# Kernel tuning notes

Hardware: AMD Instinct MI355X
Metric: run time of the kernel (lower is better)

## Reference

```python
import jax, jax.numpy as jnp
import numpy as np

H_MAX = 0.05
TIME_LEN = 5  # t = linspace(0, 1, 5); uniform segments of length 0.25
N_STEPS = int(np.ceil(0.25 / H_MAX))  # Euler steps per segment = 5 (matches torch ode_solve)


def setup_inputs() -> dict:
    key = jax.random.key(0)
    k1, k2, k3, k4, k5 = jax.random.split(key, 5)
    bs, d, hidden = 1024, 1024, 2048
    z0 = jax.random.normal(k1, (bs, d), dtype=jnp.float32)
    t = jnp.linspace(0.0, 1.0, TIME_LEN).astype(jnp.float32)
    # MLP ODEF params: f(z, t) = tanh([z, t] @ W1 + b1) @ W2 + b2
    s1 = 1.0 / np.sqrt(d + 1)
    s2 = 1.0 / np.sqrt(hidden)
    W1 = jax.random.uniform(k2, (d + 1, hidden), jnp.float32, -s1, s1)
    b1 = jax.random.uniform(k3, (hidden,), jnp.float32, -s1, s1)
    W2 = jax.random.uniform(k4, (hidden, d), jnp.float32, -s2, s2)
    b2 = jax.random.uniform(k5, (d,), jnp.float32, -s2, s2)
    return {"z0": z0, "t": t, "W1": W1, "b1": b1, "W2": W2, "b2": b2}


def _f(z, t_scalar, W1, b1, W2, b2):
    # z: [bs, d]; t_scalar broadcast as an extra input feature
    bs = z.shape[0]
    zt = jnp.concatenate([z, jnp.full((bs, 1), t_scalar, dtype=z.dtype)], axis=1)
    h = jnp.tanh(zt @ W1 + b1)
    return h @ W2 + b2


def _ode_solve(z0, t0, t1, W1, b1, W2, b2):
    # Euler: z <- z + h * f(z, t), N_STEPS fixed steps (h_max = 0.05)
    h = (t1 - t0) / N_STEPS

    def step(carry, _):
        z, t = carry
        z = z + h * _f(z, t, W1, b1, W2, b2)
        return (z, t + h), None

    (z, _), _ = jax.lax.scan(step, (z0, t0), None, length=N_STEPS)
    return z


def reference(z0, t, W1, b1, W2, b2):
    # NeuralODE.forward with return_whole_sequence=False: returns z at final time point.
    z = z0
    for i in range(TIME_LEN - 1):  # small fixed loop over time checkpoints
        z = _ode_solve(z, t[i], t[i + 1], W1, b1, W2, b2)
    return z
```

## Files before the change

kernel.cpp:

```cpp
#include <hip/hip_runtime.h>
#include <cstdint>
#include <cstddef>


typedef __bf16 bf16x8 __attribute__((ext_vector_type(8)));
typedef float f32x4 __attribute__((ext_vector_type(4)));

#define WAITV(N) asm volatile("s_waitcnt vmcnt(" #N ") lgkmcnt(0)" ::: "memory")
#define BARRIER() asm volatile("s_barrier" ::: "memory")
#define SEP() asm volatile("" ::: "memory")

__device__ __forceinline__ unsigned short f2bf(float f) {
  union { float f; unsigned u; } v; v.f = f;
  unsigned r = v.u + 0x7fffu + ((v.u >> 16) & 1u);
  return (unsigned short)(r >> 16);
}

__device__ __forceinline__ float fast_tanh(float x) {
  float e = __builtin_amdgcn_exp2f(x * 2.8853900817779268f);
  return 1.0f - 2.0f * __builtin_amdgcn_rcpf(1.0f + e);
}

__global__ void prep_all(const float* __restrict__ W1,
                         const float* __restrict__ W2,
                         unsigned short* __restrict__ W1T,
                         unsigned short* __restrict__ W2T,
                         const float* __restrict__ z0,
                         float* __restrict__ zf,
                         unsigned short* __restrict__ zbf,
                         float* __restrict__ w1l) {
  __shared__ float tile[32][33];
  const int b = blockIdx.x;
  const int tid = threadIdx.x;
  const int tx = tid & 31, ty = tid >> 5;
  if (b < 4096) {
    const bool w1 = (b < 2048);
    const float* in = w1 ? W1 : W2;
    unsigned short* out = w1 ? W1T : W2T;
    const int rows = w1 ? 1024 : 2048;
    const int cols = w1 ? 2048 : 1024;
    const int bb = w1 ? b : b - 2048;
    const int c0 = w1 ? (bb & 63) * 32 : (bb & 31) * 32;
    const int r0 = w1 ? (bb >> 6) * 32 : (bb >> 5) * 32;
#pragma unroll
    for (int j = 0; j < 32; j += 8)
      tile[ty + j][tx] = in[(size_t)(r0 + ty + j) * cols + (c0 + tx)];
    __syncthreads();
#pragma unroll
    for (int j = 0; j < 32; j += 8)
      out[(size_t)(c0 + ty + j) * rows + (r0 + tx)] = f2bf(tile[tx][ty + j]);
  } else {
    const int i = (b - 4096) * 256 + tid;
    float v = z0[i];
    zf[i] = v;
    zbf[i] = f2bf(v);
    if (i < 2048) w1l[i] = W1[(size_t)1024 * 2048 + i];
  }
}

__device__ __forceinline__ void stage64(const unsigned short* __restrict__ g,
                                        size_t ld, int row0, int k0,
                                        unsigned short* lp, int tid) {
  int r = tid >> 3;
  int c = (tid & 7) ^ (r & 7);
  __builtin_amdgcn_global_load_lds(
      (const __attribute__((address_space(1))) void*)(
          g + (size_t)(row0 + r) * ld + k0 + c * 8),
      (__attribute__((address_space(3))) void*)(lp + tid * 8), 16, 0, 0);
}

__device__ __forceinline__ bf16x8 frag_ld(const unsigned short* lp, int row,
                                          int chunk_logical, int x) {
  return *(const bf16x8*)(lp + row * 64 + ((chunk_logical ^ x) << 3));
}

__global__ __launch_bounds__(512, 1) void gemm1_kernel(
    const unsigned short* __restrict__ Zb,
    const unsigned short* __restrict__ W1T,
    unsigned short* __restrict__ H,
    const float* __restrict__ b1, const float* __restrict__ w1l, float tval) {
  __shared__ __align__(16) unsigned short lds[73728];
  const int tid = threadIdx.x;
  const int lane = tid & 63, wid = tid >> 6;
  const int l15 = lane & 15, q = lane >> 4, x = l15 & 7;
  const int bid = blockIdx.x;
  const int xcd = bid & 7, loc = bid >> 3;
  const int mt = (loc & 3) | ((xcd & 3) << 2);
  const int nt = (loc >> 2) | ((xcd >> 2) << 3);
  const int m0 = mt * 64, n0 = nt * 128;

  unsigned short* const buf0 = lds;
  unsigned short* const buf1 = lds + 24576;
  unsigned short* const buf2 = lds + 49152;

  f32x4 acc[2][2] = {};

  auto stage_tile = [&](int t, unsigned short* p) {
    int k = t * 128;
    stage64(Zb, 1024, m0, k, p, tid);
    stage64(Zb, 1024, m0, k + 64, p + 4096, tid);
    stage64(W1T, 1024, n0, k, p + 8192, tid);
    stage64(W1T, 1024, n0 + 64, k, p + 12288, tid);
    stage64(W1T, 1024, n0, k + 64, p + 16384, tid);
    stage64(W1T, 1024, n0 + 64, k + 64, p + 20480, tid);
  };
  auto compute = [&](const unsigned short* p) {
    const unsigned short* A0 = p + (wid & 1) * 2048;
    const unsigned short* B0 = p + 8192 + (wid >> 1) * 2048;
#pragma unroll
    for (int kk = 0; kk < 4; ++kk) {
      const unsigned short* A = A0 + (kk >> 1) * 4096;
      const unsigned short* B = B0 + (kk >> 1) * 8192;
      const int cb = ((kk & 1) << 2) + q;
      bf16x8 a[2], bb[2];
#pragma unroll
      for (int im = 0; im < 2; ++im)
        a[im] = frag_ld(A, im * 16 + l15, cb, x);
#pragma unroll
      for (int jn = 0; jn < 2; ++jn)
        bb[jn] = frag_ld(B, jn * 16 + l15, cb, x);
#pragma unroll
      for (int im = 0; im < 2; ++im)
#pragma unroll
        for (int jn = 0; jn < 2; ++jn)
          acc[im][jn] = __builtin_amdgcn_mfma_f32_16x16x32_bf16(
              a[im], bb[jn], acc[im][jn], 0, 0, 0);
    }
  };

#define STEP(t, pc, pn) \
  WAITV(6);             \
  BARRIER();            \
  stage_tile((t) + 2, pn); \
  compute(pc)

  stage_tile(0, buf0);
  SEP();
  stage_tile(1, buf1);

  STEP(0, buf0, buf2);
  STEP(1, buf1, buf0);
  STEP(2, buf2, buf1);
  STEP(3, buf0, buf2);
  STEP(4, buf1, buf0);
  STEP(5, buf2, buf1);
  WAITV(6);
  BARRIER();
  compute(buf0);
  WAITV(0);
  BARRIER();
  compute(buf1);
#undef STEP

#pragma unroll
  for (int jn = 0; jn < 2; ++jn) {
    int col = n0 + (wid >> 1) * 32 + jn * 16 + l15;
    float bb = b1[col] + tval * w1l[col];
#pragma unroll
    for (int im = 0; im < 2; ++im) {
      int rowb = m0 + (wid & 1) * 32 + im * 16 + q * 4;
#pragma unroll
      for (int r = 0; r < 4; ++r)
        H[(size_t)(rowb + r) * 2048 + col] =
            f2bf(fast_tanh(acc[im][jn][r] + bb));
    }
  }
}

__global__ __launch_bounds__(512, 1) void gemm2_kernel(
    const unsigned short* __restrict__ Hb,
    const unsigned short* __restrict__ W2T,
    const float* __restrict__ b2,
    const float* __restrict__ zf,
    float* __restrict__ outf,
    unsigned short* __restrict__ zbf,
    float h) {
  __shared__ __align__(16) unsigned short lds[49152];
  const int tid = threadIdx.x;
  const int lane = tid & 63, wid = tid >> 6;
  const int l15 = lane & 15, q = lane >> 4, x = l15 & 7;
  const int kh = wid >> 2, mh = (wid >> 1) & 1, nh = wid & 1;
  const int bid = blockIdx.x;
  const int xcd = bid & 7, loc = bid >> 3;
  const int mt = (loc & 3) | ((xcd & 3) << 2);
  const int nt = (loc >> 2) | ((xcd >> 2) << 3);
  const int m0 = mt * 64, n0 = nt * 64;

  unsigned short* const buf0 = lds;
  unsigned short* const buf1 = lds + 16384;
  unsigned short* const buf2 = lds + 32768;

  f32x4 acc[2][2] = {};

  auto stage_tile = [&](int t, unsigned short* p) {
    int k = t * 64;
    stage64(Hb, 2048, m0, k, p, tid);
    stage64(Hb, 2048, m0, k + 1024, p + 4096, tid);
    stage64(W2T, 2048, n0, k, p + 8192, tid);
    stage64(W2T, 2048, n0, k + 1024, p + 12288, tid);
  };
  auto compute = [&](const unsigned short* p) {
    const unsigned short* A = p + kh * 4096 + mh * 2048;
    const unsigned short* B = p + 8192 + kh * 4096 + nh * 2048;
#pragma unroll
    for (int kk = 0; kk < 2; ++kk) {
      bf16x8 a[2], bb[2];
#pragma unroll
      for (int im = 0; im < 2; ++im)
        a[im] = frag_ld(A, im * 16 + l15, (kk << 2) + q, x);
#pragma unroll
      for (int jn = 0; jn < 2; ++jn)
        bb[jn] = frag_ld(B, jn * 16 + l15, (kk << 2) + q, x);
#pragma unroll
      for (int im = 0; im < 2; ++im)
#pragma unroll
        for (int jn = 0; jn < 2; ++jn)
          acc[im][jn] = __builtin_amdgcn_mfma_f32_16x16x32_bf16(
              a[im], bb[jn], acc[im][jn], 0, 0, 0);
    }
  };

#define STEP(t, pc, pn) \
  WAITV(4);             \
  BARRIER();            \
  stage_tile((t) + 2, pn); \
  compute(pc)

  stage_tile(0, buf0);
  SEP();
  stage_tile(1, buf1);

  STEP(0, buf0, buf2);
  STEP(1, buf1, buf0);
  STEP(2, buf2, buf1);
  STEP(3, buf0, buf2);
  STEP(4, buf1, buf0);
  STEP(5, buf2, buf1);
  STEP(6, buf0, buf2);
  STEP(7, buf1, buf0);
  STEP(8, buf2, buf1);
  STEP(9, buf0, buf2);
  STEP(10, buf1, buf0);
  STEP(11, buf2, buf1);
  STEP(12, buf0, buf2);
  STEP(13, buf1, buf0);
  WAITV(4);
  BARRIER();
  compute(buf2);
  WAITV(0);
  BARRIER();
  compute(buf0);
#undef STEP

  __syncthreads();
  float* red = (float*)lds;
  const int region = (mh * 2 + nh) * 1056;
  if (kh == 1) {
#pragma unroll
    for (int im = 0; im < 2; ++im)
#pragma unroll
      for (int jn = 0; jn < 2; ++jn) {
        int c = jn * 16 + l15;
#pragma unroll
        for (int r = 0; r < 4; ++r)
          red[region + (im * 16 + q * 4 + r) * 33 + c] = acc[im][jn][r];
      }
  }
  __syncthreads();
  if (kh == 0) {
#pragma unroll
    for (int jn = 0; jn < 2; ++jn) {
      int coll = nh * 32 + jn * 16 + l15;
      int col = n0 + coll;
      float bb = b2[col];
#pragma unroll
      for (int im = 0; im < 2; ++im) {
        int rowl = im * 16 + q * 4;
#pragma unroll
        for (int r = 0; r < 4; ++r) {
          float s = acc[im][jn][r] +
                    red[region + (rowl + r) * 33 + jn * 16 + l15];
          size_t gidx = (size_t)(m0 + mh * 32 + rowl + r) * 1024 + col;
          float zv = zf[gidx] + h * (s + bb);
          outf[gidx] = zv;
          zbf[gidx] = f2bf(zv);
        }
      }
    }
  }
}

extern "C" void kernel_launch(void* const* d_in, const int* in_sizes, int n_in,
                              void* d_out, int out_size, void* d_ws,
                              size_t ws_size, hipStream_t stream) {
  const float* z0 = (const float*)d_in[0];
  const float* W1 = (const float*)d_in[2];
  const float* b1 = (const float*)d_in[3];
  const float* W2 = (const float*)d_in[4];
  const float* b2 = (const float*)d_in[5];
  float* out = (float*)d_out;

  char* ws = (char*)d_ws;
  unsigned short* W1T = (unsigned short*)(ws + 0);
  unsigned short* W2T = (unsigned short*)(ws + (4u << 20));
  unsigned short* zbf = (unsigned short*)(ws + (8u << 20));
  unsigned short* Hbf = (unsigned short*)(ws + (10u << 20));
  float* zf = (float*)(ws + (14u << 20));
  float* w1l = (float*)(ws + (18u << 20));

  prep_all<<<8192, 256, 0, stream>>>(W1, W2, W1T, W2T, z0, zf, zbf, w1l);

  const float h = 0.05f;
  for (int seg = 0; seg < 4; ++seg) {
    float tcur = 0.25f * (float)seg;
    for (int j = 0; j < 5; ++j) {
      gemm1_kernel<<<256, 512, 0, stream>>>(zbf, W1T, Hbf, b1, w1l, tcur);
      bool last = (seg == 3 && j == 4);
      float* outf = last ? out : zf;
      gemm2_kernel<<<256, 512, 0, stream>>>(Hbf, W2T, b2, zf, outf, zbf, h);
      tcur += h;
    }
  }
}
```

Measured before the change: 436.9 us.

## Store activations in MFMA-fragment order and load A operands directly from global

The bf16 copies of z and of the hidden activation H are now written in a pre-swizzled layout that matches the per-lane MFMA A-fragment order. Each GEMM then reads A fragments straight from global memory into registers instead of staging them through LDS. Only the weight tiles go through the LDS pipeline, so the LDS footprint and the staging traffic per step both shrink. The cost is scattered epilogue stores and global-load latency on the A path, which is only partly covered by the existing prefetch barrier scheme.

```diff
diff --git a/kernel.cpp b/kernel.cpp
--- a/kernel.cpp
+++ b/kernel.cpp
@@ -9,6 +9,7 @@
 #define WAITV(N) asm volatile("s_waitcnt vmcnt(" #N ") lgkmcnt(0)" ::: "memory")
 #define BARRIER() asm volatile("s_barrier" ::: "memory")
 #define SEP() asm volatile("" ::: "memory")
+#define MFMA(a, b, c) __builtin_amdgcn_mfma_f32_16x16x32_bf16(a, b, c, 0, 0, 0)
 
 __device__ __forceinline__ unsigned short f2bf(float f) {
   union { float f; unsigned u; } v; v.f = f;
@@ -53,7 +54,11 @@
     const int i = (b - 4096) * 256 + tid;
     float v = z0[i];
     zf[i] = v;
-    zbf[i] = f2bf(v);
+    const int R = i >> 10, C = i & 1023;
+    const int off = ((R >> 6) * 16 + (C >> 6)) * 4096 + ((R >> 5) & 1) * 2048 +
+                    ((C >> 5) & 1) * 1024 + ((R >> 4) & 1) * 512 +
+                    ((C >> 3) & 3) * 128 + (R & 15) * 8 + (C & 7);
+    zbf[off] = f2bf(v);
     if (i < 2048) w1l[i] = W1[(size_t)1024 * 2048 + i];
   }
 }
@@ -79,90 +84,101 @@
     const unsigned short* __restrict__ W1T,
     unsigned short* __restrict__ H,
     const float* __restrict__ b1, const float* __restrict__ w1l, float tval) {
-  __shared__ __align__(16) unsigned short lds[73728];
+  __shared__ __align__(16) unsigned short lds[24576];
   const int tid = threadIdx.x;
   const int lane = tid & 63, wid = tid >> 6;
   const int l15 = lane & 15, q = lane >> 4, x = l15 & 7;
+  const int mh = wid & 1, nq = wid >> 1;
   const int bid = blockIdx.x;
   const int xcd = bid & 7, loc = bid >> 3;
   const int mt = (loc & 3) | ((xcd & 3) << 2);
   const int nt = (loc >> 2) | ((xcd >> 2) << 3);
-  const int m0 = mt * 64, n0 = nt * 128;
+  const int n0 = nt * 128;
 
   unsigned short* const buf0 = lds;
-  unsigned short* const buf1 = lds + 24576;
-  unsigned short* const buf2 = lds + 49152;
+  unsigned short* const buf1 = lds + 8192;
+  unsigned short* const buf2 = lds + 16384;
 
   f32x4 acc[2][2] = {};
 
+  const unsigned short* const Af = Zb + (size_t)(mt * 16) * 4096 + mh * 2048 + lane * 8;
+
   auto stage_tile = [&](int t, unsigned short* p) {
-    int k = t * 128;
-    stage64(Zb, 1024, m0, k, p, tid);
-    stage64(Zb, 1024, m0, k + 64, p + 4096, tid);
-    stage64(W1T, 1024, n0, k, p + 8192, tid);
-    stage64(W1T, 1024, n0 + 64, k, p + 12288, tid);
-    stage64(W1T, 1024, n0, k + 64, p + 16384, tid);
-    stage64(W1T, 1024, n0 + 64, k + 64, p + 20480, tid);
+    int k = t * 64;
+    stage64(W1T, 1024, n0, k, p, tid);
+    stage64(W1T, 1024, n0 + 64, k, p + 4096, tid);
   };
-  auto compute = [&](const unsigned short* p) {
-    const unsigned short* A0 = p + (wid & 1) * 2048;
-    const unsigned short* B0 = p + 8192 + (wid >> 1) * 2048;
-#pragma unroll
-    for (int kk = 0; kk < 4; ++kk) {
-      const unsigned short* A = A0 + (kk >> 1) * 4096;
-      const unsigned short* B = B0 + (kk >> 1) * 8192;
-      const int cb = ((kk & 1) << 2) + q;
-      bf16x8 a[2], bb[2];
-#pragma unroll
-      for (int im = 0; im < 2; ++im)
-        a[im] = frag_ld(A, im * 16 + l15, cb, x);
-#pragma unroll
-      for (int jn = 0; jn < 2; ++jn)
-        bb[jn] = frag_ld(B, jn * 16 + l15, cb, x);
-#pragma unroll
-      for (int im = 0; im < 2; ++im)
-#pragma unroll
-        for (int jn = 0; jn < 2; ++jn)
-          acc[im][jn] = __builtin_amdgcn_mfma_f32_16x16x32_bf16(
-              a[im], bb[jn], acc[im][jn], 0, 0, 0);
-    }
+  auto compute = [&](const unsigned short* p, bf16x8 a00, bf16x8 a01,
+                     bf16x8 a10, bf16x8 a11) {
+    const unsigned short* B = p + nq * 2048;
+    bf16x8 b0 = frag_ld(B, l15, q, x);
+    bf16x8 b1v = frag_ld(B, 16 + l15, q, x);
+    acc[0][0] = MFMA(a00, b0, acc[0][0]);
+    acc[0][1] = MFMA(a00, b1v, acc[0][1]);
+    acc[1][0] = MFMA(a01, b0, acc[1][0]);
+    acc[1][1] = MFMA(a01, b1v, acc[1][1]);
+    bf16x8 b2 = frag_ld(B, l15, 4 + q, x);
+    bf16x8 b3 = frag_ld(B, 16 + l15, 4 + q, x);
+    acc[0][0] = MFMA(a10, b2, acc[0][0]);
+    acc[0][1] = MFMA(a10, b3, acc[0][1]);
+    acc[1][0] = MFMA(a11, b2, acc[1][0]);
+    acc[1][1] = MFMA(a11, b3, acc[1][1]);
   };
 
-#define STEP(t, pc, pn) \
-  WAITV(6);             \
-  BARRIER();            \
-  stage_tile((t) + 2, pn); \
-  compute(pc)
+#define STEP(t, pc, pn, W)                              \
+  {                                                     \
+    WAITV(W);                                           \
+    BARRIER();                                          \
+    const unsigned short* Ab = Af + (t) * 4096;         \
+    bf16x8 a00 = *(const bf16x8*)(Ab);                  \
+    bf16x8 a01 = *(const bf16x8*)(Ab + 512);            \
+    bf16x8 a10 = *(const bf16x8*)(Ab + 1024);           \
+    bf16x8 a11 = *(const bf16x8*)(Ab + 1536);           \
+    SEP();                                              \
+    if ((t) < 14) stage_tile((t) + 2, pn);              \
+    compute(pc, a00, a01, a10, a11);                    \
+  }
 
   stage_tile(0, buf0);
   SEP();
   stage_tile(1, buf1);
 
-  STEP(0, buf0, buf2);
-  STEP(1, buf1, buf0);
-  STEP(2, buf2, buf1);
-  STEP(3, buf0, buf2);
-  STEP(4, buf1, buf0);
-  STEP(5, buf2, buf1);
-  WAITV(6);
-  BARRIER();
-  compute(buf0);
-  WAITV(0);
-  BARRIER();
-  compute(buf1);
+  STEP(0, buf0, buf2, 2);
+  STEP(1, buf1, buf0, 2);
+  STEP(2, buf2, buf1, 2);
+  STEP(3, buf0, buf2, 2);
+  STEP(4, buf1, buf0, 2);
+  STEP(5, buf2, buf1, 2);
+  STEP(6, buf0, buf2, 2);
+  STEP(7, buf1, buf0, 2);
+  STEP(8, buf2, buf1, 2);
+  STEP(9, buf0, buf2, 2);
+  STEP(10, buf1, buf0, 2);
+  STEP(11, buf2, buf1, 2);
+  STEP(12, buf0, buf2, 2);
+  STEP(13, buf1, buf0, 2);
+  STEP(14, buf2, buf1, 2);
+  STEP(15, buf0, buf1, 0);
 #undef STEP
 
-#pragma unroll
-  for (int jn = 0; jn < 2; ++jn) {
-    int col = n0 + (wid >> 1) * 32 + jn * 16 + l15;
-    float bb = b1[col] + tval * w1l[col];
-#pragma unroll
-    for (int im = 0; im < 2; ++im) {
-      int rowb = m0 + (wid & 1) * 32 + im * 16 + q * 4;
-#pragma unroll
-      for (int r = 0; r < 4; ++r)
-        H[(size_t)(rowb + r) * 2048 + col] =
-            f2bf(fast_tanh(acc[im][jn][r] + bb));
+  {
+    const int laneoff = (l15 >> 3) * 128 + q * 32 + (l15 & 7);
+#pragma unroll
+    for (int jn = 0; jn < 2; ++jn) {
+      const int colb = n0 + nq * 32 + jn * 16;
+      const int col = colb + l15;
+      const float bb = b1[col] + tval * w1l[col];
+      const int kh2 = colb >> 10;
+      const int c10 = colb & 1023;
+      const int t2 = c10 >> 6;
+      const int ckb = (c10 >> 3) & 7;
+      const int fb = ((mt * 2 + kh2) * 16 + t2) * 4096 + mh * 2048 +
+                     (ckb >> 2) * 1024 + (ckb & 3) * 128 + laneoff;
+#pragma unroll
+      for (int im = 0; im < 2; ++im)
+#pragma unroll
+        for (int r = 0; r < 4; ++r)
+          H[fb + im * 512 + r * 8] = f2bf(fast_tanh(acc[im][jn][r] + bb));
     }
   }
 }
@@ -175,7 +191,7 @@
     float* __restrict__ outf,
     unsigned short* __restrict__ zbf,
     float h) {
-  __shared__ __align__(16) unsigned short lds[49152];
+  __shared__ __align__(16) unsigned short lds[24576];
   const int tid = threadIdx.x;
   const int lane = tid & 63, wid = tid >> 6;
   const int l15 = lane & 15, q = lane >> 4, x = l15 & 7;
@@ -187,69 +203,70 @@
   const int m0 = mt * 64, n0 = nt * 64;
 
   unsigned short* const buf0 = lds;
-  unsigned short* const buf1 = lds + 16384;
-  unsigned short* const buf2 = lds + 32768;
+  unsigned short* const buf1 = lds + 8192;
+  unsigned short* const buf2 = lds + 16384;
 
   f32x4 acc[2][2] = {};
+
+  const unsigned short* const Af =
+      Hb + (size_t)((mt * 2 + kh) * 16) * 4096 + mh * 2048 + lane * 8;
 
   auto stage_tile = [&](int t, unsigned short* p) {
     int k = t * 64;
-    stage64(Hb, 2048, m0, k, p, tid);
-    stage64(Hb, 2048, m0, k + 1024, p + 4096, tid);
-    stage64(W2T, 2048, n0, k, p + 8192, tid);
-    stage64(W2T, 2048, n0, k + 1024, p + 12288, tid);
+    stage64(W2T, 2048, n0, k, p, tid);
+    stage64(W2T, 2048, n0, k + 1024, p + 4096, tid);
   };
-  auto compute = [&](const unsigned short* p) {
-    const unsigned short* A = p + kh * 4096 + mh * 2048;
-    const unsigned short* B = p + 8192 + kh * 4096 + nh * 2048;
-#pragma unroll
-    for (int kk = 0; kk < 2; ++kk) {
-      bf16x8 a[2], bb[2];
-#pragma unroll
-      for (int im = 0; im < 2; ++im)
-        a[im] = frag_ld(A, im * 16 + l15, (kk << 2) + q, x);
-#pragma unroll
-      for (int jn = 0; jn < 2; ++jn)
-        bb[jn] = frag_ld(B, jn * 16 + l15, (kk << 2) + q, x);
-#pragma unroll
-      for (int im = 0; im < 2; ++im)
-#pragma unroll
-        for (int jn = 0; jn < 2; ++jn)
-          acc[im][jn] = __builtin_amdgcn_mfma_f32_16x16x32_bf16(
-              a[im], bb[jn], acc[im][jn], 0, 0, 0);
-    }
+  auto compute = [&](const unsigned short* p, bf16x8 a00, bf16x8 a01,
+                     bf16x8 a10, bf16x8 a11) {
+    const unsigned short* B = p + kh * 4096 + nh * 2048;
+    bf16x8 b0 = frag_ld(B, l15, q, x);
+    bf16x8 b1v = frag_ld(B, 16 + l15, q, x);
+    acc[0][0] = MFMA(a00, b0, acc[0][0]);
+    acc[0][1] = MFMA(a00, b1v, acc[0][1]);
+    acc[1][0] = MFMA(a01, b0, acc[1][0]);
+    acc[1][1] = MFMA(a01, b1v, acc[1][1]);
+    bf16x8 b2 = frag_ld(B, l15, 4 + q, x);
+    bf16x8 b3 = frag_ld(B, 16 + l15, 4 + q, x);
+    acc[0][0] = MFMA(a10, b2, acc[0][0]);
+    acc[0][1] = MFMA(a10, b3, acc[0][1]);
+    acc[1][0] = MFMA(a11, b2, acc[1][0]);
+    acc[1][1] = MFMA(a11, b3, acc[1][1]);
   };
 
-#define STEP(t, pc, pn) \
-  WAITV(4);             \
-  BARRIER();            \
-  stage_tile((t) + 2, pn); \
-  compute(pc)
+#define STEP(t, pc, pn, W)                              \
+  {                                                     \
+    WAITV(W);                                           \
+    BARRIER();                                          \
+    const unsigned short* Ab = Af + (t) * 4096;         \
+    bf16x8 a00 = *(const bf16x8*)(Ab);                  \
+    bf16x8 a01 = *(const bf16x8*)(Ab + 512);            \
+    bf16x8 a10 = *(const bf16x8*)(Ab + 1024);           \
+    bf16x8 a11 = *(const bf16x8*)(Ab + 1536);           \
+    SEP();                                              \
+    if ((t) < 14) stage_tile((t) + 2, pn);              \
+    compute(pc, a00, a01, a10, a11);                    \
+  }
 
   stage_tile(0, buf0);
   SEP();
   stage_tile(1, buf1);
 
-  STEP(0, buf0, buf2);
-  STEP(1, buf1, buf0);
-  STEP(2, buf2, buf1);
-  STEP(3, buf0, buf2);
-  STEP(4, buf1, buf0);
-  STEP(5, buf2, buf1);
-  STEP(6, buf0, buf2);
-  STEP(7, buf1, buf0);
-  STEP(8, buf2, buf1);
-  STEP(9, buf0, buf2);
-  STEP(10, buf1, buf0);
-  STEP(11, buf2, buf1);
-  STEP(12, buf0, buf2);
-  STEP(13, buf1, buf0);
-  WAITV(4);
-  BARRIER();
-  compute(buf2);
-  WAITV(0);
-  BARRIER();
-  compute(buf0);
+  STEP(0, buf0, buf2, 2);
+  STEP(1, buf1, buf0, 2);
+  STEP(2, buf2, buf1, 2);
+  STEP(3, buf0, buf2, 2);
+  STEP(4, buf1, buf0, 2);
+  STEP(5, buf2, buf1, 2);
+  STEP(6, buf0, buf2, 2);
+  STEP(7, buf1, buf0, 2);
+  STEP(8, buf2, buf1, 2);
+  STEP(9, buf0, buf2, 2);
+  STEP(10, buf1, buf0, 2);
+  STEP(11, buf2, buf1, 2);
+  STEP(12, buf0, buf2, 2);
+  STEP(13, buf1, buf0, 2);
+  STEP(14, buf2, buf1, 2);
+  STEP(15, buf0, buf1, 0);
 #undef STEP
 
   __syncthreads();
@@ -268,14 +285,19 @@
   }
   __syncthreads();
   if (kh == 0) {
+    const int laneoff = (l15 >> 3) * 128 + q * 32 + (l15 & 7);
 #pragma unroll
     for (int jn = 0; jn < 2; ++jn) {
-      int coll = nh * 32 + jn * 16 + l15;
-      int col = n0 + coll;
-      float bb = b2[col];
+      const int colb = n0 + nh * 32 + jn * 16;
+      const int col = colb + l15;
+      const float bb = b2[col];
+      const int t1 = colb >> 6;
+      const int ckb = (colb >> 3) & 7;
+      const int fb = (mt * 16 + t1) * 4096 + mh * 2048 +
+                     (ckb >> 2) * 1024 + (ckb & 3) * 128 + laneoff;
 #pragma unroll
       for (int im = 0; im < 2; ++im) {
-        int rowl = im * 16 + q * 4;
+        const int rowl = im * 16 + q * 4;
 #pragma unroll
         for (int r = 0; r < 4; ++r) {
           float s = acc[im][jn][r] +
@@ -283,7 +305,7 @@
           size_t gidx = (size_t)(m0 + mh * 32 + rowl + r) * 1024 + col;
           float zv = zf[gidx] + h * (s + bb);
           outf[gidx] = zv;
-          zbf[gidx] = f2bf(zv);
+          zbf[fb + im * 512 + r * 8] = f2bf(zv);
         }
       }
     }
```

Measured after the change: 665.6 us. 1.52x slower.

## Fuse all Euler steps into one persistent cooperative kernel with flag sync

Applied to the files above, without the earlier changes.

Replaces the 40 separate GEMM kernel launches with a single cooperative persistent kernel of 256 blocks that loops over all 20 Euler steps. Blocks synchronize through per-tile release/acquire flags on row-blocks instead of kernel boundaries. Each block prefetches weight tiles before spinning on the flags, so weight loads overlap the wait. GEMM1 is retiled from 128-wide to 64-wide K stages so it fits the smaller shared LDS buffer. This targets launch overhead and the tail idle at each kernel boundary, at the cost of spin-wait traffic and any load imbalance between dependent tiles.

```diff
diff --git a/kernel.cpp b/kernel.cpp
--- a/kernel.cpp
+++ b/kernel.cpp
@@ -28,7 +28,8 @@
                          const float* __restrict__ z0,
                          float* __restrict__ zf,
                          unsigned short* __restrict__ zbf,
-                         float* __restrict__ w1l) {
+                         float* __restrict__ w1l,
+                         int* __restrict__ flg) {
   __shared__ float tile[32][33];
   const int b = blockIdx.x;
   const int tid = threadIdx.x;
@@ -55,6 +56,7 @@
     zf[i] = v;
     zbf[i] = f2bf(v);
     if (i < 2048) w1l[i] = W1[(size_t)1024 * 2048 + i];
+    if (i < 512) flg[i] = 0;
   }
 }
 
@@ -74,12 +76,19 @@
   return *(const bf16x8*)(lp + row * 64 + ((chunk_logical ^ x) << 3));
 }
 
-__global__ __launch_bounds__(512, 1) void gemm1_kernel(
-    const unsigned short* __restrict__ Zb,
+__global__ __launch_bounds__(512, 1) void ode_fused(
     const unsigned short* __restrict__ W1T,
-    unsigned short* __restrict__ H,
-    const float* __restrict__ b1, const float* __restrict__ w1l, float tval) {
-  __shared__ __align__(16) unsigned short lds[73728];
+    const unsigned short* __restrict__ W2T,
+    const float* __restrict__ b1,
+    const float* __restrict__ b2,
+    const float* __restrict__ w1l,
+    unsigned short* __restrict__ zbf,
+    unsigned short* __restrict__ Hbf,
+    float* __restrict__ zf,
+    float* __restrict__ out,
+    int* __restrict__ flg1,
+    int* __restrict__ flg2) {
+  __shared__ __align__(16) unsigned short lds[49152];
   const int tid = threadIdx.x;
   const int lane = tid & 63, wid = tid >> 6;
   const int l15 = lane & 15, q = lane >> 4, x = l15 & 7;
@@ -87,206 +96,241 @@
   const int xcd = bid & 7, loc = bid >> 3;
   const int mt = (loc & 3) | ((xcd & 3) << 2);
   const int nt = (loc >> 2) | ((xcd >> 2) << 3);
-  const int m0 = mt * 64, n0 = nt * 128;
-
-  unsigned short* const buf0 = lds;
-  unsigned short* const buf1 = lds + 24576;
-  unsigned short* const buf2 = lds + 49152;
-
-  f32x4 acc[2][2] = {};
-
-  auto stage_tile = [&](int t, unsigned short* p) {
-    int k = t * 128;
-    stage64(Zb, 1024, m0, k, p, tid);
-    stage64(Zb, 1024, m0, k + 64, p + 4096, tid);
-    stage64(W1T, 1024, n0, k, p + 8192, tid);
-    stage64(W1T, 1024, n0 + 64, k, p + 12288, tid);
-    stage64(W1T, 1024, n0, k + 64, p + 16384, tid);
-    stage64(W1T, 1024, n0 + 64, k + 64, p + 20480, tid);
-  };
-  auto compute = [&](const unsigned short* p) {
-    const unsigned short* A0 = p + (wid & 1) * 2048;
-    const unsigned short* B0 = p + 8192 + (wid >> 1) * 2048;
-#pragma unroll
-    for (int kk = 0; kk < 4; ++kk) {
-      const unsigned short* A = A0 + (kk >> 1) * 4096;
-      const unsigned short* B = B0 + (kk >> 1) * 8192;
-      const int cb = ((kk & 1) << 2) + q;
-      bf16x8 a[2], bb[2];
-#pragma unroll
-      for (int im = 0; im < 2; ++im)
-        a[im] = frag_ld(A, im * 16 + l15, cb, x);
-#pragma unroll
-      for (int jn = 0; jn < 2; ++jn)
-        bb[jn] = frag_ld(B, jn * 16 + l15, cb, x);
-#pragma unroll
-      for (int im = 0; im < 2; ++im)
-#pragma unroll
-        for (int jn = 0; jn < 2; ++jn)
-          acc[im][jn] = __builtin_amdgcn_mfma_f32_16x16x32_bf16(
-              a[im], bb[jn], acc[im][jn], 0, 0, 0);
+  const int m0 = mt * 64;
+  const int n0g1 = nt * 128, n0g2 = nt * 64;
+  const int g1mh = wid & 1, g1nq = wid >> 1;
+  const int kh = wid >> 2, g2mh = (wid >> 1) & 1, g2nh = wid & 1;
+  const float h = 0.05f;
+
+  float tcur = 0.0f;
+#pragma unroll 1
+  for (int s = 0; s < 20; ++s) {
+    if ((s % 5) == 0) tcur = 0.25f * (float)(s / 5);
+
+    {
+      unsigned short* const c0 = lds;
+      unsigned short* const c1 = lds + 12288;
+      unsigned short* const c2 = lds + 24576;
+      f32x4 acc[2][2] = {};
+
+      auto stageB = [&](int t, unsigned short* p) {
+        int k = t * 64;
+        stage64(W1T, 1024, n0g1, k, p + 4096, tid);
+        stage64(W1T, 1024, n0g1 + 64, k, p + 8192, tid);
+      };
+      auto stageA = [&](int t, unsigned short* p) {
+        stage64(zbf, 1024, m0, t * 64, p, tid);
+      };
+      auto stage_tile = [&](int t, unsigned short* p) { stageA(t, p); stageB(t, p); };
+      auto compute = [&](const unsigned short* p) {
+        const unsigned short* A = p + g1mh * 2048;
+        const unsigned short* B = p + 4096 + g1nq * 2048;
+#pragma unroll
+        for (int kk = 0; kk < 2; ++kk) {
+          bf16x8 a[2], bb[2];
+#pragma unroll
+          for (int im = 0; im < 2; ++im)
+            a[im] = frag_ld(A, im * 16 + l15, (kk << 2) + q, x);
+#pragma unroll
+          for (int jn = 0; jn < 2; ++jn)
+            bb[jn] = frag_ld(B, jn * 16 + l15, (kk << 2) + q, x);
+#pragma unroll
+          for (int im = 0; im < 2; ++im)
+#pragma unroll
+            for (int jn = 0; jn < 2; ++jn)
+              acc[im][jn] = __builtin_amdgcn_mfma_f32_16x16x32_bf16(
+                  a[im], bb[jn], acc[im][jn], 0, 0, 0);
+        }
+      };
+
+      __syncthreads();
+      stageB(0, c0);
+      SEP();
+      stageB(1, c1);
+      if (wid == 0) {
+        const int j = lane & 15;
+        while (__hip_atomic_load(&flg2[mt * 16 + j], __ATOMIC_RELAXED,
+                                 __HIP_MEMORY_SCOPE_AGENT) < s)
+          __builtin_amdgcn_s_sleep(2);
+        __threadfence();
+      }
+      __syncthreads();
+      stageA(0, c0);
+      SEP();
+      stageA(1, c1);
+
+#define STEP1(t, pc, pn, W) \
+      WAITV(W);             \
+      BARRIER();            \
+      stage_tile((t) + 2, pn); \
+      compute(pc)
+
+      STEP1(0, c0, c2, 1);
+      STEP1(1, c1, c0, 3);
+      STEP1(2, c2, c1, 3);
+      STEP1(3, c0, c2, 3);
+      STEP1(4, c1, c0, 3);
+      STEP1(5, c2, c1, 3);
+      STEP1(6, c0, c2, 3);
+      STEP1(7, c1, c0, 3);
+      STEP1(8, c2, c1, 3);
+      STEP1(9, c0, c2, 3);
+      STEP1(10, c1, c0, 3);
+      STEP1(11, c2, c1, 3);
+      STEP1(12, c0, c2, 3);
+      STEP1(13, c1, c0, 3);
+      WAITV(3);
+      BARRIER();
+      compute(c2);
+      WAITV(0);
+      BARRIER();
+      compute(c0);
+#undef STEP1
+
+#pragma unroll
+      for (int jn = 0; jn < 2; ++jn) {
+        int col = n0g1 + g1nq * 32 + jn * 16 + l15;
+        float bb = b1[col] + tcur * w1l[col];
+#pragma unroll
+        for (int im = 0; im < 2; ++im) {
+          int rowb = m0 + g1mh * 32 + im * 16 + q * 4;
+#pragma unroll
+          for (int r = 0; r < 4; ++r)
+            Hbf[(size_t)(rowb + r) * 2048 + col] =
+                f2bf(fast_tanh(acc[im][jn][r] + bb));
+        }
+      }
+      __syncthreads();
+      if (tid == 0)
+        __hip_atomic_store(&flg1[mt * 16 + nt], s + 1, __ATOMIC_RELEASE,
+                           __HIP_MEMORY_SCOPE_AGENT);
     }
-  };
-
-#define STEP(t, pc, pn) \
-  WAITV(6);             \
-  BARRIER();            \
-  stage_tile((t) + 2, pn); \
-  compute(pc)
-
-  stage_tile(0, buf0);
-  SEP();
-  stage_tile(1, buf1);
-
-  STEP(0, buf0, buf2);
-  STEP(1, buf1, buf0);
-  STEP(2, buf2, buf1);
-  STEP(3, buf0, buf2);
-  STEP(4, buf1, buf0);
-  STEP(5, buf2, buf1);
-  WAITV(6);
-  BARRIER();
-  compute(buf0);
-  WAITV(0);
-  BARRIER();
-  compute(buf1);
-#undef STEP
-
-#pragma unroll
-  for (int jn = 0; jn < 2; ++jn) {
-    int col = n0 + (wid >> 1) * 32 + jn * 16 + l15;
-    float bb = b1[col] + tval * w1l[col];
-#pragma unroll
-    for (int im = 0; im < 2; ++im) {
-      int rowb = m0 + (wid & 1) * 32 + im * 16 + q * 4;
-#pragma unroll
-      for (int r = 0; r < 4; ++r)
-        H[(size_t)(rowb + r) * 2048 + col] =
-            f2bf(fast_tanh(acc[im][jn][r] + bb));
+
+    {
+      unsigned short* const c0 = lds;
+      unsigned short* const c1 = lds + 16384;
+      unsigned short* const c2 = lds + 32768;
+      f32x4 acc[2][2] = {};
+
+      auto stageB = [&](int t, unsigned short* p) {
+        int k = t * 64;
+        stage64(W2T, 2048, n0g2, k, p + 8192, tid);
+        stage64(W2T, 2048, n0g2, k + 1024, p + 12288, tid);
+      };
+      auto stageA = [&](int t, unsigned short* p) {
+        int k = t * 64;
+        stage64(Hbf, 2048, m0, k, p, tid);
+        stage64(Hbf, 2048, m0, k + 1024, p + 4096, tid);
+      };
+      auto stage_tile = [&](int t, unsigned short* p) { stageA(t, p); stageB(t, p); };
+      auto compute = [&](const unsigned short* p) {
+        const unsigned short* A = p + kh * 4096 + g2mh * 2048;
+        const unsigned short* B = p + 8192 + kh * 4096 + g2nh * 2048;
+#pragma unroll
+        for (int kk = 0; kk < 2; ++kk) {
+          bf16x8 a[2], bb[2];
+#pragma unroll
+          for (int im = 0; im < 2; ++im)
+            a[im] = frag_ld(A, im * 16 + l15, (kk << 2) + q, x);
+#pragma unroll
+          for (int jn = 0; jn < 2; ++jn)
+            bb[jn] = frag_ld(B, jn * 16 + l15, (kk << 2) + q, x);
+#pragma unroll
+          for (int im = 0; im < 2; ++im)
+#pragma unroll
+            for (int jn = 0; jn < 2; ++jn)
+              acc[im][jn] = __builtin_amdgcn_mfma_f32_16x16x32_bf16(
+                  a[im], bb[jn], acc[im][jn], 0, 0, 0);
+        }
+      };
+
+      __syncthreads();
+      stageB(0, c0);
+      SEP();
+      stageB(1, c1);
+      if (wid == 0) {
+        const int j = lane & 15;
+        while (__hip_atomic_load(&flg1[mt * 16 + j], __ATOMIC_RELAXED,
+                                 __HIP_MEMORY_SCOPE_AGENT) < s + 1)
+          __builtin_amdgcn_s_sleep(2);
+        __threadfence();
+      }
+      __syncthreads();
+      stageA(0, c0);
+      SEP();
+      stageA(1, c1);
+
+#define STEP2(t, pc, pn, W) \
+      WAITV(W);             \
+      BARRIER();            \
+      stage_tile((t) + 2, pn); \
+      compute(pc)
+
+      STEP2(0, c0, c2, 2);
+      STEP2(1, c1, c0, 4);
+      STEP2(2, c2, c1, 4);
+      STEP2(3, c0, c2, 4);
+      STEP2(4, c1, c0, 4);
+      STEP2(5, c2, c1, 4);
+      STEP2(6, c0, c2, 4);
+      STEP2(7, c1, c0, 4);
+      STEP2(8, c2, c1, 4);
+      STEP2(9, c0, c2, 4);
+      STEP2(10, c1, c0, 4);
+      STEP2(11, c2, c1, 4);
+      STEP2(12, c0, c2, 4);
+      STEP2(13, c1, c0, 4);
+      WAITV(4);
+      BARRIER();
+      compute(c2);
+      WAITV(0);
+      BARRIER();
+      compute(c0);
+#undef STEP2
+
+      __syncthreads();
+      float* red = (float*)lds;
+      const int region = (g2mh * 2 + g2nh) * 1056;
+      if (kh == 1) {
+#pragma unroll
+        for (int im = 0; im < 2; ++im)
+#pragma unroll
+          for (int jn = 0; jn < 2; ++jn) {
+            int c = jn * 16 + l15;
+#pragma unroll
+            for (int r = 0; r < 4; ++r)
+              red[region + (im * 16 + q * 4 + r) * 33 + c] = acc[im][jn][r];
+          }
+      }
+      __syncthreads();
+      float* const outp = (s == 19) ? out : zf;
+      if (kh == 0) {
+#pragma unroll
+        for (int jn = 0; jn < 2; ++jn) {
+          int col = n0g2 + g2nh * 32 + jn * 16 + l15;
+          float bb = b2[col];
+#pragma unroll
+          for (int im = 0; im < 2; ++im) {
+            int rowl = im * 16 + q * 4;
+#pragma unroll
+            for (int r = 0; r < 4; ++r) {
+              float sum = acc[im][jn][r] +
+                          red[region + (rowl + r) * 33 + jn * 16 + l15];
+              size_t gidx = (size_t)(m0 + g2mh * 32 + rowl + r) * 1024 + col;
+              float zv = zf[gidx] + h * (sum + bb);
+              outp[gidx] = zv;
+              zbf[gidx] = f2bf(zv);
+            }
+          }
+        }
+      }
+      __syncthreads();
+      if (tid == 0)
+        __hip_atomic_store(&flg2[mt * 16 + nt], s + 1, __ATOMIC_RELEASE,
+                           __HIP_MEMORY_SCOPE_AGENT);
     }
-  }
-}
-
-__global__ __launch_bounds__(512, 1) void gemm2_kernel(
-    const unsigned short* __restrict__ Hb,
-    const unsigned short* __restrict__ W2T,
-    const float* __restrict__ b2,
-    const float* __restrict__ zf,
-    float* __restrict__ outf,
-    unsigned short* __restrict__ zbf,
-    float h) {
-  __shared__ __align__(16) unsigned short lds[49152];
-  const int tid = threadIdx.x;
-  const int lane = tid & 63, wid = tid >> 6;
-  const int l15 = lane & 15, q = lane >> 4, x = l15 & 7;
-  const int kh = wid >> 2, mh = (wid >> 1) & 1, nh = wid & 1;
-  const int bid = blockIdx.x;
-  const int xcd = bid & 7, loc = bid >> 3;
-  const int mt = (loc & 3) | ((xcd & 3) << 2);
-  const int nt = (loc >> 2) | ((xcd >> 2) << 3);
-  const int m0 = mt * 64, n0 = nt * 64;
-
-  unsigned short* const buf0 = lds;
-  unsigned short* const buf1 = lds + 16384;
-  unsigned short* const buf2 = lds + 32768;
-
-  f32x4 acc[2][2] = {};
-
-  auto stage_tile = [&](int t, unsigned short* p) {
-    int k = t * 64;
-    stage64(Hb, 2048, m0, k, p, tid);
-    stage64(Hb, 2048, m0, k + 1024, p + 4096, tid);
-    stage64(W2T, 2048, n0, k, p + 8192, tid);
-    stage64(W2T, 2048, n0, k + 1024, p + 12288, tid);
-  };
-  auto compute = [&](const unsigned short* p) {
-    const unsigned short* A = p + kh * 4096 + mh * 2048;
-    const unsigned short* B = p + 8192 + kh * 4096 + nh * 2048;
-#pragma unroll
-    for (int kk = 0; kk < 2; ++kk) {
-      bf16x8 a[2], bb[2];
-#pragma unroll
-      for (int im = 0; im < 2; ++im)
-        a[im] = frag_ld(A, im * 16 + l15, (kk << 2) + q, x);
-#pragma unroll
-      for (int jn = 0; jn < 2; ++jn)
-        bb[jn] = frag_ld(B, jn * 16 + l15, (kk << 2) + q, x);
-#pragma unroll
-      for (int im = 0; im < 2; ++im)
-#pragma unroll
-        for (int jn = 0; jn < 2; ++jn)
-          acc[im][jn] = __builtin_amdgcn_mfma_f32_16x16x32_bf16(
-              a[im], bb[jn], acc[im][jn], 0, 0, 0);
-    }
-  };
-
-#define STEP(t, pc, pn) \
-  WAITV(4);             \
-  BARRIER();            \
-  stage_tile((t) + 2, pn); \
-  compute(pc)
-
-  stage_tile(0, buf0);
-  SEP();
-  stage_tile(1, buf1);
-
-  STEP(0, buf0, buf2);
-  STEP(1, buf1, buf0);
-  STEP(2, buf2, buf1);
-  STEP(3, buf0, buf2);
-  STEP(4, buf1, buf0);
-  STEP(5, buf2, buf1);
-  STEP(6, buf0, buf2);
-  STEP(7, buf1, buf0);
-  STEP(8, buf2, buf1);
-  STEP(9, buf0, buf2);
-  STEP(10, buf1, buf0);
-  STEP(11, buf2, buf1);
-  STEP(12, buf0, buf2);
-  STEP(13, buf1, buf0);
-  WAITV(4);
-  BARRIER();
-  compute(buf2);
-  WAITV(0);
-  BARRIER();
-  compute(buf0);
-#undef STEP
-
-  __syncthreads();
-  float* red = (float*)lds;
-  const int region = (mh * 2 + nh) * 1056;
-  if (kh == 1) {
-#pragma unroll
-    for (int im = 0; im < 2; ++im)
-#pragma unroll
-      for (int jn = 0; jn < 2; ++jn) {
-        int c = jn * 16 + l15;
-#pragma unroll
-        for (int r = 0; r < 4; ++r)
-          red[region + (im * 16 + q * 4 + r) * 33 + c] = acc[im][jn][r];
-      }
-  }
-  __syncthreads();
-  if (kh == 0) {
-#pragma unroll
-    for (int jn = 0; jn < 2; ++jn) {
-      int coll = nh * 32 + jn * 16 + l15;
-      int col = n0 + coll;
-      float bb = b2[col];
-#pragma unroll
-      for (int im = 0; im < 2; ++im) {
-        int rowl = im * 16 + q * 4;
-#pragma unroll
-        for (int r = 0; r < 4; ++r) {
-          float s = acc[im][jn][r] +
-                    red[region + (rowl + r) * 33 + jn * 16 + l15];
-          size_t gidx = (size_t)(m0 + mh * 32 + rowl + r) * 1024 + col;
-          float zv = zf[gidx] + h * (s + bb);
-          outf[gidx] = zv;
-          zbf[gidx] = f2bf(zv);
-        }
-      }
-    }
+
+    tcur += h;
   }
 }
 
@@ -307,18 +351,14 @@
   unsigned short* Hbf = (unsigned short*)(ws + (10u << 20));
   float* zf = (float*)(ws + (14u << 20));
   float* w1l = (float*)(ws + (18u << 20));
-
-  prep_all<<<8192, 256, 0, stream>>>(W1, W2, W1T, W2T, z0, zf, zbf, w1l);
-
-  const float h = 0.05f;
-  for (int seg = 0; seg < 4; ++seg) {
-    float tcur = 0.25f * (float)seg;
-    for (int j = 0; j < 5; ++j) {
-      gemm1_kernel<<<256, 512, 0, stream>>>(zbf, W1T, Hbf, b1, w1l, tcur);
-      bool last = (seg == 3 && j == 4);
-      float* outf = last ? out : zf;
-      gemm2_kernel<<<256, 512, 0, stream>>>(Hbf, W2T, b2, zf, outf, zbf, h);
-      tcur += h;
-    }
-  }
-}
+  int* flg = (int*)(ws + (19u << 20));
+  int* flg1 = flg;
+  int* flg2 = flg + 256;
+
+  prep_all<<<8192, 256, 0, stream>>>(W1, W2, W1T, W2T, z0, zf, zbf, w1l, flg);
+
+  void* args[] = {&W1T, &W2T, (void*)&b1, (void*)&b2, &w1l,
+                  &zbf, &Hbf, &zf, &out, &flg1, &flg2};
+  hipLaunchCooperativeKernel((void*)ode_fused, dim3(256), dim3(512), args, 0,
+                             stream);
+}
```

Result: slower. 1.384 ms (+216.9%).
